# Optimization experiments

Hardware: AMD Instinct MI355X
Metric: run time of the kernel (lower is better)

The kernel has to match this reference:

```python
import jax, jax.numpy as jnp
import numpy as np

SLOPE = (1.0 / 8 + 1.0 / 3) / 2  # F.rrelu in eval mode: mean of (lower, upper)
DILS = [1, 2, 4, 8, 16]
WINDOW = 32
TEMP = 0.1


def rrelu(x):
    return jnp.where(x >= 0, x, x * SLOPE)


def conv1d(x, w, b, dil):
    # x: [B, Cin, T], w: [Cout, Cin, K]
    y = jax.lax.conv_general_dilated(x, w, window_strides=(1,), padding='VALID',
                                     rhs_dilation=(dil,),
                                     dimension_numbers=('NCH', 'OIH', 'NCH'))
    return y + b[None, :, None]


def setup_inputs() -> dict:
    key = jax.random.key(0)
    ks = jax.random.split(key, 32)
    B, T, R, K, W = 16, 16384, 8, 2, WINDOW
    ins = [1, 64, 64, 64, 64]
    outs = [64, 64, 64, 64, R]
    inp = {"x": jax.random.normal(ks[0], (B, 1, T), jnp.float32)}
    for l in range(5):
        inp[f"cw{l}"] = jax.random.normal(ks[1 + l], (outs[l], ins[l], K), jnp.float32) * 0.1
        inp[f"cb{l}"] = jax.random.normal(ks[6 + l], (outs[l],), jnp.float32) * 0.1
    pc = [(2 * R, 2 * R), (2 * R, 2 * R), (1, 2 * R)]  # params_convs, kernel 1
    for i, (o, ci) in enumerate(pc):
        inp[f"mw{i}"] = jax.random.normal(ks[11 + i], (o, ci, 1), jnp.float32) * 0.1
        inp[f"mb{i}"] = jax.random.normal(ks[14 + i], (o,), jnp.float32) * 0.1
    inp["sqrt_cov_tt"] = jax.random.uniform(ks[17], (R, 1), jnp.float32)
    inp["fish_jt"] = jax.random.normal(ks[18], (R, W), jnp.float32) * 0.01
    u = jax.random.uniform(ks[19], (B, T, R), jnp.float32, minval=1e-6, maxval=1.0 - 1e-6)
    inp["gumbel"] = -jnp.log(-jnp.log(u))
    return inp


def reference(x, cw0, cb0, cw1, cb1, cw2, cb2, cw3, cb3, cw4, cb4,
              mw0, mb0, mw1, mb1, mw2, mb2, sqrt_cov_tt, fish_jt, gumbel):
    pad = sum(DILS)
    T = x.shape[-1]
    W = WINDOW
    # forward_pass: causal dilated conv stack with rrelu
    h = jnp.pad(x, ((0, 0), (0, 0), (pad, 0)))
    for w, b, d in zip([cw0, cw1, cw2, cw3, cw4], [cb0, cb1, cb2, cb3, cb4], DILS):
        h = rrelu(conv1d(h, w, b, d))
    # h: [B, R, T]
    logits = jnp.transpose(h, (0, 2, 1))  # [B, T, R]
    gen_z = jax.nn.softmax((logits + gumbel) / TEMP, axis=-1)
    gen_z = jnp.transpose(gen_z, (0, 2, 1))  # [B, R, T]
    # params_convs (1x1 convs): conv -> (rrelu, conv) x2
    m = conv1d(jnp.concatenate([gen_z, h], axis=1), mw0, mb0, 1)
    m = conv1d(rrelu(m), mw1, mb1, 1)
    mus = conv1d(rrelu(m), mw2, mb2, 1)  # [B, 1, T]
    cov_tt = jnp.einsum('brt,rl->blt', gen_z, sqrt_cov_tt) ** 2  # [B, 1, T]
    cov_tt = cov_tt[:, :, W:T]  # [B, 1, T-W]
    fj = jnp.einsum('brt,rw->bwt', gen_z, fish_jt)[:, :, W:T]  # [B, W, T-W]
    # vectorized sliding window: x_window[b, j, t] = x[b, 0, t + j]
    idx = jnp.arange(W)[:, None] + jnp.arange(T - W)[None, :]  # [W, T-W]
    xw = x[:, 0, :][:, idx]   # [B, W, T-W]
    mw_ = mus[:, 0, :][:, idx]  # [B, W, T-W]
    _mus = mus[:, 0, W:T] - jnp.einsum('bwt,bwt->bt', cov_tt * fj, xw - mw_)
    return (_mus, gen_z)
```

## Files before the change

kernel.cpp:

```cpp
#include <hip/hip_runtime.h>
#include <hip/hip_bf16.h>

#define NT 512
#define TS 160
#define TC 192
#define NTILE 103
#define PBA 222
#define PBB 220
#define NB 16
#define T_ 16384
#define W_ 32
#define TW_ (T_ - W_)
#define SLOPE_C 0.22916666666666666f

#define WIMG_W4   49152
#define WIMG_CST  53248
#define WIMG_USH  56320

typedef short v8s __attribute__((ext_vector_type(8)));
typedef float v4f __attribute__((ext_vector_type(4)));

__device__ __forceinline__ float rr(float v){ return v >= 0.f ? v : v * SLOPE_C; }
__device__ __forceinline__ ushort f2bs(float f){ __hip_bfloat16 h = __float2bfloat16(f); return *(ushort*)&h; }
__device__ __forceinline__ float bs2f(ushort u){ union{unsigned i; float f;} v; v.i = ((unsigned)u) << 16; return v.f; }

__device__ __forceinline__ int agr(int p, int gi){ return p*128 + ((gi ^ (p & 15)) << 3); }
__device__ __forceinline__ int widx(int wr, int ci){
  return wr*64 + ((((ci >> 3) ^ (wr & 7)) << 3) | (ci & 7));
}

__global__ __launch_bounds__(256) void kW(
    const float* __restrict__ cw1, const float* __restrict__ cw2,
    const float* __restrict__ cw3, const float* __restrict__ cw4,
    const float* __restrict__ cw0, const float* __restrict__ cb0,
    const float* __restrict__ cb1, const float* __restrict__ cb2,
    const float* __restrict__ cb3, const float* __restrict__ cb4,
    const float* __restrict__ mw0, const float* __restrict__ mb0,
    const float* __restrict__ mw1, const float* __restrict__ mb1,
    const float* __restrict__ mw2, const float* __restrict__ mb2,
    const float* __restrict__ fish, const float* __restrict__ sct,
    ushort* __restrict__ wimg)
{
  const int id = blockIdx.x*256 + threadIdx.x;
  if (id < 24576){
    int l = id >> 13, e = id & 8191;
    const float* src = (l == 0) ? cw1 : ((l == 1) ? cw2 : cw3);
    int c = e >> 7, rem = e & 127, ci = rem >> 1, k = rem & 1;
    float v = src[e];
    ushort h = f2bs(v), lo = f2bs(v - bs2f(h));
    int ix = widx(k*64 + c, ci);
    wimg[l*16384 + ix] = h;
    wimg[l*16384 + 8192 + ix] = lo;
  } else if (id < 25600){
    int e = id - 24576;
    int c = e >> 7, rem = e & 127, ci = rem >> 1, k = rem & 1;
    float v = cw4[e];
    ushort h = f2bs(v), lo = f2bs(v - bs2f(h));
    int ix = widx(k*16 + c, ci);
    wimg[WIMG_W4 + ix] = h;
    wimg[WIMG_W4 + 2048 + ix] = lo;
  } else if (id < 27648){
    int e = id - 25600;
    int pl = e >> 10, rem = e & 1023, k = rem >> 9, r2 = rem & 511;
    int m = 8 + (r2 >> 6), ci = r2 & 63;
    wimg[WIMG_W4 + pl*2048 + widx(k*16 + m, ci)] = 0;
  } else if (id < 29184){
    int e = id - 27648;
    float v = 0.f;
    if      (e < 256)  v = mw0[e];
    else if (e < 512)  v = mw1[e - 256];
    else if (e < 528)  v = mw2[e - 512];
    else if (e < 544)  v = mb0[e - 528];
    else if (e < 560)  v = mb1[e - 544];
    else if (e < 561)  v = mb2[0];
    else if (e >= 576 && e < 584)  v = cb4[e - 576];
    else if (e >= 592 && e < 720)  v = cw0[e - 592];
    else if (e >= 720 && e < 784)  v = cb0[e - 720];
    else if (e >= 784 && e < 848)  v = cb1[e - 784];
    else if (e >= 848 && e < 912)  v = cb2[e - 848];
    else if (e >= 912 && e < 976)  v = cb3[e - 912];
    else if (e >= 1024 && e < 1280) v = fish[e - 1024];
    else if (e >= 1280 && e < 1288) v = sct[e - 1280];
    ((float*)(wimg + WIMG_CST))[e] = v;
  }
}

template<int D, int NSRC, int NDST>
__device__ __forceinline__ void mfma_layer(const ushort* __restrict__ src,
    ushort* __restrict__ dst, const ushort* __restrict__ wlds,
    const float* __restrict__ cbias, int tid)
{
  const int wave = tid >> 6;
  if (wave >= 7) return;
  const int lane = tid & 63;
  const int n = lane & 15, quad = lane >> 4;
  const int p0 = wave * 32;

  v4f acc[8];
  const v4f vz = {0.f, 0.f, 0.f, 0.f};
#pragma unroll
  for (int i = 0; i < 8; ++i) acc[i] = vz;

#pragma unroll
  for (int tap = 0; tap < 2; ++tap){
#pragma unroll
    for (int kb = 0; kb < 2; ++kb){
      const int kg = kb*4 + quad;
      v8s wh[4], wl[4], ah[2], al[2];
#pragma unroll
      for (int mt = 0; mt < 4; ++mt){
        int wr = tap*64 + mt*16 + n;
        int base = wr*64 + ((kg ^ (wr & 7)) << 3);
        wh[mt] = *(const v8s*)(wlds + base);
        wl[mt] = *(const v8s*)(wlds + 8192 + base);
      }
#pragma unroll
      for (int nt = 0; nt < 2; ++nt){
        int p = p0 + nt*16 + n + tap*D;
        if (p >= NSRC) p = NSRC - 1;
        ah[nt] = *(const v8s*)(src + agr(p, kg));
        al[nt] = *(const v8s*)(src + agr(p, 8 + kg));
      }
#pragma unroll
      for (int nt = 0; nt < 2; ++nt)
#pragma unroll
        for (int mt = 0; mt < 4; ++mt){
          v4f a = acc[nt*4 + mt];
          a = __builtin_amdgcn_mfma_f32_16x16x32_bf16(wh[mt], ah[nt], a, 0, 0, 0);
          a = __builtin_amdgcn_mfma_f32_16x16x32_bf16(wh[mt], al[nt], a, 0, 0, 0);
          a = __builtin_amdgcn_mfma_f32_16x16x32_bf16(wl[mt], ah[nt], a, 0, 0, 0);
          acc[nt*4 + mt] = a;
        }
    }
  }

#pragma unroll
  for (int nt = 0; nt < 2; ++nt){
    int p = p0 + nt*16 + n;
    if (p < NDST){
#pragma unroll
      for (int mt = 0; mt < 4; ++mt){
#pragma unroll
        for (int r = 0; r < 4; r += 2){
          int c = mt*16 + quad*4 + r;
          float y0 = rr(acc[nt*4 + mt][r]     + cbias[c]);
          float y1 = rr(acc[nt*4 + mt][r + 1] + cbias[c + 1]);
          ushort h0 = f2bs(y0), h1 = f2bs(y1);
          ushort l0 = f2bs(y0 - bs2f(h0)), l1 = f2bs(y1 - bs2f(h1));
          int gh = agr(p, c >> 3)       + (c & 7);
          int gl = agr(p, 8 + (c >> 3)) + (c & 7);
          *(unsigned*)(dst + gh) = (unsigned)h0 | ((unsigned)h1 << 16);
          *(unsigned*)(dst + gl) = (unsigned)l0 | ((unsigned)l1 << 16);
        }
      }
    }
  }
}

__global__ __launch_bounds__(NT) void kAB(
    const float* __restrict__ x, const float* __restrict__ gum,
    const ushort* __restrict__ wimg,
    float* __restrict__ out0, float* __restrict__ out_gz)
{
  __shared__ __align__(16) ushort bufA[PBA*128];
  __shared__ __align__(16) ushort bufB[PBB*128];
  __shared__ __align__(16) ushort wlds[16384];
  __shared__ __align__(16) ushort w4lds[4096];
  __shared__ __align__(16) float  cstl[1536];

  float* xbuf = (float*)bufB;
  float*  fA   = (float*)bufA;
  float*  h4s  = fA;
  float*  musl = fA + 1536;
  float*  pacc = fA + 1728;
  float*  xg   = fA + 2240;
  ushort* zl   = (ushort*)(fA + 2464);

  const int tile = blockIdx.x, b = blockIdx.y;
  const int o0 = tile * TS;
  const int core = (T_ - o0 < TC) ? (T_ - o0) : TC;
  const int ncut = (TW_ - o0 < TS) ? (TW_ - o0) : TS;
  const int tid = threadIdx.x;

  const int nx = core + 31;
  for (int i = tid; i < nx; i += NT){
    int g = o0 + i;
    xbuf[i] = (g >= 31) ? x[(size_t)b*T_ + g - 31] : 0.f;
  }
  for (int i = tid; i < 2048; i += NT)
    *(v8s*)(wlds + i*8) = *(const v8s*)(wimg + i*8);
  for (int i = tid; i < 512; i += NT)
    *(v8s*)(w4lds + i*8) = *(const v8s*)(wimg + WIMG_W4 + i*8);
  for (int i = tid; i < 768; i += NT)
    ((float2*)cstl)[i] = ((const float2*)(wimg + WIMG_CST))[i];
  __syncthreads();

  {
    const int n0 = core + 30;
    for (int i = tid; i < PBA*32; i += NT){
      int p = i >> 5, c = (i & 31)*2;
      float y0 = 0.f, y1 = 0.f;
      if (p < n0){
        float xp = xbuf[p], xq = xbuf[p + 1];
        y0 = rr(cstl[720 + c]     + cstl[592 + 2*c]*xp     + cstl[593 + 2*c]*xq);
        y1 = rr(cstl[720 + c + 1] + cstl[594 + 2*c]*xp     + cstl[595 + 2*c]*xq);
      }
      ushort h0 = f2bs(y0), h1 = f2bs(y1);
      ushort l0 = f2bs(y0 - bs2f(h0)), l1 = f2bs(y1 - bs2f(h1));
      *(unsigned*)(bufA + agr(p, c >> 3)       + (c & 7)) = (unsigned)h0 | ((unsigned)h1 << 16);
      *(unsigned*)(bufA + agr(p, 8 + (c >> 3)) + (c & 7)) = (unsigned)l0 | ((unsigned)l1 << 16);
    }
  }
  __syncthreads();

  mfma_layer<2, PBA, PBB>(bufA, bufB, wlds, cstl + 784, tid);
  __syncthreads();
  for (int i = tid; i < 2048; i += NT)
    *(v8s*)(wlds + i*8) = *(const v8s*)(wimg + 16384 + i*8);
  __syncthreads();
  mfma_layer<4, PBB, PBA>(bufB, bufA, wlds, cstl + 848, tid);
  __syncthreads();
  for (int i = tid; i < 2048; i += NT)
    *(v8s*)(wlds + i*8) = *(const v8s*)(wimg + 32768 + i*8);
  __syncthreads();
  mfma_layer<8, PBA, PBB>(bufA, bufB, wlds, cstl + 912, tid);
  __syncthreads();

  {
    const int wave = tid >> 6;
    if (wave < 7){
      const int lane = tid & 63;
      const int n = lane & 15, quad = lane >> 4;
      const int p0 = wave * 32;
      v4f acc2[2];
      const v4f vz = {0.f, 0.f, 0.f, 0.f};
      acc2[0] = vz; acc2[1] = vz;
#pragma unroll
      for (int tap = 0; tap < 2; ++tap){
#pragma unroll
        for (int kb = 0; kb < 2; ++kb){
          const int kg = kb*4 + quad;
          int wr = tap*16 + n;
          int base = wr*64 + ((kg ^ (wr & 7)) << 3);
          v8s wh = *(const v8s*)(w4lds + base);
          v8s wl = *(const v8s*)(w4lds + 2048 + base);
#pragma unroll
          for (int nt = 0; nt < 2; ++nt){
            int p = p0 + nt*16 + n + tap*16;
            if (p >= PBB) p = PBB - 1;
            v8s ah = *(const v8s*)(bufB + agr(p, kg));
            v8s al = *(const v8s*)(bufB + agr(p, 8 + kg));
            v4f a = acc2[nt];
            a = __builtin_amdgcn_mfma_f32_16x16x32_bf16(wh, ah, a, 0, 0, 0);
            a = __builtin_amdgcn_mfma_f32_16x16x32_bf16(wh, al, a, 0, 0, 0);
            a = __builtin_amdgcn_mfma_f32_16x16x32_bf16(wl, ah, a, 0, 0, 0);
            acc2[nt] = a;
          }
        }
      }
#pragma unroll
      for (int nt = 0; nt < 2; ++nt){
        int p = p0 + nt*16 + n;
        if (p < core && quad < 2){
#pragma unroll
          for (int r = 0; r < 4; ++r){
            int c = quad*4 + r;
            h4s[c*TC + p] = rr(acc2[nt][r] + cstl[576 + c]);
          }
        }
      }
    }
  }
  __syncthreads();

  if (tid < core){
    const int j = tid, t = o0 + j;
    float l[8];
#pragma unroll
    for (int r = 0; r < 8; ++r) l[r] = h4s[r*TC + j];
    float gv[8];
    *(float4*)&gv[0] = *(const float4*)(gum + (size_t)(b*T_ + t)*8);
    *(float4*)&gv[4] = *(const float4*)(gum + (size_t)(b*T_ + t)*8 + 4);
    float s[8], mx = -1e30f;
#pragma unroll
    for (int r = 0; r < 8; ++r){ s[r] = (l[r] + gv[r]) * 10.0f; mx = fmaxf(mx, s[r]); }
    float e[8], sum = 0.f;
#pragma unroll
    for (int r = 0; r < 8; ++r){ e[r] = __expf(s[r] - mx); sum += e[r]; }
    float inv = 1.0f / sum;
    float z[8];
#pragma unroll
    for (int r = 0; r < 8; ++r){
      z[r] = e[r] * inv;
      out_gz[(size_t)(b*8 + r)*T_ + t] = z[r];
    }
#pragma unroll
    for (int r = 0; r < 8; r += 2)
      *(unsigned*)(zl + j*8 + r) = (unsigned)f2bs(z[r]) | ((unsigned)f2bs(z[r+1]) << 16);
    float m0[16];
#pragma unroll
    for (int o = 0; o < 16; ++o){
      float a = cstl[528 + o];
#pragma unroll
      for (int i = 0; i < 8; ++i) a += cstl[o*16 + i] * z[i];
#pragma unroll
      for (int i = 0; i < 8; ++i) a += cstl[o*16 + 8 + i] * l[i];
      m0[o] = rr(a);
    }
    float m1[16];
#pragma unroll
    for (int o = 0; o < 16; ++o){
      float a = cstl[544 + o];
#pragma unroll
      for (int i = 0; i < 16; ++i) a += cstl[256 + o*16 + i] * m0[i];
      m1[o] = rr(a);
    }
    float mu = cstl[560];
#pragma unroll
    for (int i = 0; i < 16; ++i) mu += cstl[512 + i] * m1[i];
    musl[j] = mu;
  } else if (tid >= 256 && tid < 480){
    int k = tid - 256;
    int g = o0 + k;
    xg[k] = (g < T_) ? x[(size_t)b*T_ + g] : 0.f;
  }
  __syncthreads();

  {
    const int h = tid >> 8, i = tid & 255;
    if (i < ncut){
      float z[8];
      v8s zv = *(const v8s*)(zl + (i + 32)*8);
#pragma unroll
      for (int r = 0; r < 8; ++r) z[r] = bs2f((ushort)zv[r]);
      float acc = 0.f;
      const int w0 = h*16;
#pragma unroll
      for (int w = 0; w < 16; ++w){
        float fj = 0.f;
#pragma unroll
        for (int r = 0; r < 8; ++r) fj += z[r] * cstl[1024 + r*32 + w0 + w];
        acc += fj * (xg[i + w0 + w] - musl[i + w0 + w]);
      }
      pacc[h*256 + i] = acc;
    }
  }
  __syncthreads();

  if (tid < ncut){
    const int i = tid;
    float z[8];
    v8s zv = *(const v8s*)(zl + (i + 32)*8);
#pragma unroll
    for (int r = 0; r < 8; ++r) z[r] = bs2f((ushort)zv[r]);
    float cv = 0.f;
#pragma unroll
    for (int r = 0; r < 8; ++r) cv += cstl[1280 + r] * z[r];
    cv *= cv;
    float acc = pacc[i] + pacc[256 + i];
    out0[(size_t)b*TW_ + o0 + i] = musl[i + 32] - cv * acc;
  }
}

extern "C" void kernel_launch(void* const* d_in, const int* in_sizes, int n_in,
                              void* d_out, int out_size, void* d_ws, size_t ws_size,
                              hipStream_t stream)
{
  const float* x   = (const float*)d_in[0];
  const float* cw0 = (const float*)d_in[1];
  const float* cb0 = (const float*)d_in[2];
  const float* cw1 = (const float*)d_in[3];
  const float* cb1 = (const float*)d_in[4];
  const float* cw2 = (const float*)d_in[5];
  const float* cb2 = (const float*)d_in[6];
  const float* cw3 = (const float*)d_in[7];
  const float* cb3 = (const float*)d_in[8];
  const float* cw4 = (const float*)d_in[9];
  const float* cb4 = (const float*)d_in[10];
  const float* mw0 = (const float*)d_in[11];
  const float* mb0 = (const float*)d_in[12];
  const float* mw1 = (const float*)d_in[13];
  const float* mb1 = (const float*)d_in[14];
  const float* mw2 = (const float*)d_in[15];
  const float* mb2 = (const float*)d_in[16];
  const float* sct = (const float*)d_in[17];
  const float* fish= (const float*)d_in[18];
  const float* gum = (const float*)d_in[19];

  float* out0   = (float*)d_out;
  float* out_gz = out0 + NB*TW_;
  ushort* wimg  = (ushort*)d_ws;

  kW<<<114, 256, 0, stream>>>(cw1, cw2, cw3, cw4, cw0, cb0, cb1, cb2, cb3, cb4,
                              mw0, mb0, mw1, mb1, mw2, mb2, fish, sct, wimg);

  dim3 gA(NTILE, NB);
  kAB<<<gA, NT, 0, stream>>>(x, gum, wimg, out0, out_gz);
}
```

Before: 249.7 us.

## Split fused kernel into conv/softmax kernel and separate sliding-window kernel, smaller tiles

The single fused kernel is split in two. The first runs the conv stack, softmax and 1x1 MLP on smaller 96-step tiles with 256 threads, reads conv weights straight from global memory instead of staging them in LDS, and writes mus to workspace. A second kernel does the 32-wide sliding-window correction, reading gen_z and mus from global memory. This lowers LDS use, cuts halo overhead per tile and raises occupancy, at the cost of an extra launch, a global round-trip for mus and gen_z, and unswizzled global weight loads. The halo grows relative to tile size, so redundant conv work increases.

```diff
diff --git a/kernel.cpp b/kernel.cpp
--- a/kernel.cpp
+++ b/kernel.cpp
@@ -1,12 +1,11 @@
 #include <hip/hip_runtime.h>
 #include <hip/hip_bf16.h>
 
-#define NT 512
-#define TS 160
-#define TC 192
-#define NTILE 103
-#define PBA 222
-#define PBB 220
+#define NT 256
+#define TT 96
+#define NTILE 171
+#define PBA 126
+#define PBB 124
 #define NB 16
 #define T_ 16384
 #define W_ 32
@@ -25,9 +24,6 @@
 __device__ __forceinline__ float bs2f(ushort u){ union{unsigned i; float f;} v; v.i = ((unsigned)u) << 16; return v.f; }
 
 __device__ __forceinline__ int agr(int p, int gi){ return p*128 + ((gi ^ (p & 15)) << 3); }
-__device__ __forceinline__ int widx(int wr, int ci){
-  return wr*64 + ((((ci >> 3) ^ (wr & 7)) << 3) | (ci & 7));
-}
 
 __global__ __launch_bounds__(256) void kW(
     const float* __restrict__ cw1, const float* __restrict__ cw2,
@@ -48,7 +44,7 @@
     int c = e >> 7, rem = e & 127, ci = rem >> 1, k = rem & 1;
     float v = src[e];
     ushort h = f2bs(v), lo = f2bs(v - bs2f(h));
-    int ix = widx(k*64 + c, ci);
+    int ix = (k*64 + c)*64 + ci;
     wimg[l*16384 + ix] = h;
     wimg[l*16384 + 8192 + ix] = lo;
   } else if (id < 25600){
@@ -56,14 +52,14 @@
     int c = e >> 7, rem = e & 127, ci = rem >> 1, k = rem & 1;
     float v = cw4[e];
     ushort h = f2bs(v), lo = f2bs(v - bs2f(h));
-    int ix = widx(k*16 + c, ci);
+    int ix = (k*16 + c)*64 + ci;
     wimg[WIMG_W4 + ix] = h;
     wimg[WIMG_W4 + 2048 + ix] = lo;
   } else if (id < 27648){
     int e = id - 25600;
     int pl = e >> 10, rem = e & 1023, k = rem >> 9, r2 = rem & 511;
     int m = 8 + (r2 >> 6), ci = r2 & 63;
-    wimg[WIMG_W4 + pl*2048 + widx(k*16 + m, ci)] = 0;
+    wimg[WIMG_W4 + pl*2048 + (k*16 + m)*64 + ci] = 0;
   } else if (id < 29184){
     int e = id - 27648;
     float v = 0.f;
@@ -87,11 +83,10 @@
 
 template<int D, int NSRC, int NDST>
 __device__ __forceinline__ void mfma_layer(const ushort* __restrict__ src,
-    ushort* __restrict__ dst, const ushort* __restrict__ wlds,
+    ushort* __restrict__ dst, const ushort* __restrict__ wg,
     const float* __restrict__ cbias, int tid)
 {
   const int wave = tid >> 6;
-  if (wave >= 7) return;
   const int lane = tid & 63;
   const int n = lane & 15, quad = lane >> 4;
   const int p0 = wave * 32;
@@ -109,10 +104,9 @@
       v8s wh[4], wl[4], ah[2], al[2];
 #pragma unroll
       for (int mt = 0; mt < 4; ++mt){
-        int wr = tap*64 + mt*16 + n;
-        int base = wr*64 + ((kg ^ (wr & 7)) << 3);
-        wh[mt] = *(const v8s*)(wlds + base);
-        wl[mt] = *(const v8s*)(wlds + 8192 + base);
+        int base = (tap*64 + mt*16 + n)*64 + kg*8;
+        wh[mt] = *(const v8s*)(wg + base);
+        wl[mt] = *(const v8s*)(wg + 8192 + base);
       }
 #pragma unroll
       for (int nt = 0; nt < 2; ++nt){
@@ -147,39 +141,29 @@
           float y1 = rr(acc[nt*4 + mt][r + 1] + cbias[c + 1]);
           ushort h0 = f2bs(y0), h1 = f2bs(y1);
           ushort l0 = f2bs(y0 - bs2f(h0)), l1 = f2bs(y1 - bs2f(h1));
-          int gh = agr(p, c >> 3)       + (c & 7);
-          int gl = agr(p, 8 + (c >> 3)) + (c & 7);
-          *(unsigned*)(dst + gh) = (unsigned)h0 | ((unsigned)h1 << 16);
-          *(unsigned*)(dst + gl) = (unsigned)l0 | ((unsigned)l1 << 16);
+          *(unsigned*)(dst + agr(p, c >> 3)       + (c & 7)) = (unsigned)h0 | ((unsigned)h1 << 16);
+          *(unsigned*)(dst + agr(p, 8 + (c >> 3)) + (c & 7)) = (unsigned)l0 | ((unsigned)l1 << 16);
         }
       }
     }
   }
 }
 
-__global__ __launch_bounds__(NT) void kAB(
+__global__ __launch_bounds__(NT, 2) void kA(
     const float* __restrict__ x, const float* __restrict__ gum,
     const ushort* __restrict__ wimg,
-    float* __restrict__ out0, float* __restrict__ out_gz)
+    float* __restrict__ ws_mus, float* __restrict__ out_gz)
 {
   __shared__ __align__(16) ushort bufA[PBA*128];
   __shared__ __align__(16) ushort bufB[PBB*128];
-  __shared__ __align__(16) ushort wlds[16384];
-  __shared__ __align__(16) ushort w4lds[4096];
   __shared__ __align__(16) float  cstl[1536];
 
   float* xbuf = (float*)bufB;
-  float*  fA   = (float*)bufA;
-  float*  h4s  = fA;
-  float*  musl = fA + 1536;
-  float*  pacc = fA + 1728;
-  float*  xg   = fA + 2240;
-  ushort* zl   = (ushort*)(fA + 2464);
+  float* h4s  = (float*)bufA;
 
   const int tile = blockIdx.x, b = blockIdx.y;
-  const int o0 = tile * TS;
-  const int core = (T_ - o0 < TC) ? (T_ - o0) : TC;
-  const int ncut = (TW_ - o0 < TS) ? (TW_ - o0) : TS;
+  const int o0 = tile * TT;
+  const int core = (T_ - o0 < TT) ? (T_ - o0) : TT;
   const int tid = threadIdx.x;
 
   const int nx = core + 31;
@@ -187,10 +171,6 @@
     int g = o0 + i;
     xbuf[i] = (g >= 31) ? x[(size_t)b*T_ + g - 31] : 0.f;
   }
-  for (int i = tid; i < 2048; i += NT)
-    *(v8s*)(wlds + i*8) = *(const v8s*)(wimg + i*8);
-  for (int i = tid; i < 512; i += NT)
-    *(v8s*)(w4lds + i*8) = *(const v8s*)(wimg + WIMG_W4 + i*8);
   for (int i = tid; i < 768; i += NT)
     ((float2*)cstl)[i] = ((const float2*)(wimg + WIMG_CST))[i];
   __syncthreads();
@@ -202,8 +182,8 @@
       float y0 = 0.f, y1 = 0.f;
       if (p < n0){
         float xp = xbuf[p], xq = xbuf[p + 1];
-        y0 = rr(cstl[720 + c]     + cstl[592 + 2*c]*xp     + cstl[593 + 2*c]*xq);
-        y1 = rr(cstl[720 + c + 1] + cstl[594 + 2*c]*xp     + cstl[595 + 2*c]*xq);
+        y0 = rr(cstl[720 + c]     + cstl[592 + 2*c]*xp + cstl[593 + 2*c]*xq);
+        y1 = rr(cstl[720 + c + 1] + cstl[594 + 2*c]*xp + cstl[595 + 2*c]*xq);
       }
       ushort h0 = f2bs(y0), h1 = f2bs(y1);
       ushort l0 = f2bs(y0 - bs2f(h0)), l1 = f2bs(y1 - bs2f(h1));
@@ -213,60 +193,53 @@
   }
   __syncthreads();
 
-  mfma_layer<2, PBA, PBB>(bufA, bufB, wlds, cstl + 784, tid);
-  __syncthreads();
-  for (int i = tid; i < 2048; i += NT)
-    *(v8s*)(wlds + i*8) = *(const v8s*)(wimg + 16384 + i*8);
-  __syncthreads();
-  mfma_layer<4, PBB, PBA>(bufB, bufA, wlds, cstl + 848, tid);
-  __syncthreads();
-  for (int i = tid; i < 2048; i += NT)
-    *(v8s*)(wlds + i*8) = *(const v8s*)(wimg + 32768 + i*8);
-  __syncthreads();
-  mfma_layer<8, PBA, PBB>(bufA, bufB, wlds, cstl + 912, tid);
+  mfma_layer<2, PBA, PBB>(bufA, bufB, wimg,         cstl + 784, tid);
+  __syncthreads();
+  mfma_layer<4, PBB, 120>(bufB, bufA, wimg + 16384, cstl + 848, tid);
+  __syncthreads();
+  mfma_layer<8, 120, 112>(bufA, bufB, wimg + 32768, cstl + 912, tid);
   __syncthreads();
 
   {
+    const ushort* wg4 = wimg + WIMG_W4;
     const int wave = tid >> 6;
-    if (wave < 7){
-      const int lane = tid & 63;
-      const int n = lane & 15, quad = lane >> 4;
-      const int p0 = wave * 32;
-      v4f acc2[2];
-      const v4f vz = {0.f, 0.f, 0.f, 0.f};
-      acc2[0] = vz; acc2[1] = vz;
-#pragma unroll
-      for (int tap = 0; tap < 2; ++tap){
-#pragma unroll
-        for (int kb = 0; kb < 2; ++kb){
-          const int kg = kb*4 + quad;
-          int wr = tap*16 + n;
-          int base = wr*64 + ((kg ^ (wr & 7)) << 3);
-          v8s wh = *(const v8s*)(w4lds + base);
-          v8s wl = *(const v8s*)(w4lds + 2048 + base);
-#pragma unroll
-          for (int nt = 0; nt < 2; ++nt){
-            int p = p0 + nt*16 + n + tap*16;
-            if (p >= PBB) p = PBB - 1;
-            v8s ah = *(const v8s*)(bufB + agr(p, kg));
-            v8s al = *(const v8s*)(bufB + agr(p, 8 + kg));
-            v4f a = acc2[nt];
-            a = __builtin_amdgcn_mfma_f32_16x16x32_bf16(wh, ah, a, 0, 0, 0);
-            a = __builtin_amdgcn_mfma_f32_16x16x32_bf16(wh, al, a, 0, 0, 0);
-            a = __builtin_amdgcn_mfma_f32_16x16x32_bf16(wl, ah, a, 0, 0, 0);
-            acc2[nt] = a;
-          }
+    const int lane = tid & 63;
+    const int n = lane & 15, quad = lane >> 4;
+    const int p0 = wave * 32;
+    v4f acc2[2];
+    const v4f vz = {0.f, 0.f, 0.f, 0.f};
+    acc2[0] = vz; acc2[1] = vz;
+#pragma unroll
+    for (int tap = 0; tap < 2; ++tap){
+#pragma unroll
+      for (int kb = 0; kb < 2; ++kb){
+        const int kg = kb*4 + quad;
+        int base = (tap*16 + n)*64 + kg*8;
+        v8s wh = *(const v8s*)(wg4 + base);
+        v8s wl = *(const v8s*)(wg4 + 2048 + base);
+#pragma unroll
+        for (int nt = 0; nt < 2; ++nt){
+          int p = p0 + nt*16 + n + tap*16;
+          if (p >= 112) p = 111;
+          v8s ah = *(const v8s*)(bufB + agr(p, kg));
+          v8s al = *(const v8s*)(bufB + agr(p, 8 + kg));
+          v4f a = acc2[nt];
+          a = __builtin_amdgcn_mfma_f32_16x16x32_bf16(wh, ah, a, 0, 0, 0);
+          a = __builtin_amdgcn_mfma_f32_16x16x32_bf16(wh, al, a, 0, 0, 0);
+          a = __builtin_amdgcn_mfma_f32_16x16x32_bf16(wl, ah, a, 0, 0, 0);
+          acc2[nt] = a;
         }
       }
-#pragma unroll
-      for (int nt = 0; nt < 2; ++nt){
-        int p = p0 + nt*16 + n;
-        if (p < core && quad < 2){
-#pragma unroll
-          for (int r = 0; r < 4; ++r){
-            int c = quad*4 + r;
-            h4s[c*TC + p] = rr(acc2[nt][r] + cstl[576 + c]);
-          }
+    }
+    __syncthreads();
+#pragma unroll
+    for (int nt = 0; nt < 2; ++nt){
+      int p = p0 + nt*16 + n;
+      if (p < core && quad < 2){
+#pragma unroll
+        for (int r = 0; r < 4; ++r){
+          int c = quad*4 + r;
+          h4s[c*TT + p] = rr(acc2[nt][r] + cstl[576 + c]);
         }
       }
     }
@@ -274,10 +247,10 @@
   __syncthreads();
 
   if (tid < core){
-    const int j = tid, t = o0 + j;
+    const int t = o0 + tid;
     float l[8];
 #pragma unroll
-    for (int r = 0; r < 8; ++r) l[r] = h4s[r*TC + j];
+    for (int r = 0; r < 8; ++r) l[r] = h4s[r*TT + tid];
     float gv[8];
     *(float4*)&gv[0] = *(const float4*)(gum + (size_t)(b*T_ + t)*8);
     *(float4*)&gv[4] = *(const float4*)(gum + (size_t)(b*T_ + t)*8 + 4);
@@ -294,9 +267,6 @@
       z[r] = e[r] * inv;
       out_gz[(size_t)(b*8 + r)*T_ + t] = z[r];
     }
-#pragma unroll
-    for (int r = 0; r < 8; r += 2)
-      *(unsigned*)(zl + j*8 + r) = (unsigned)f2bs(z[r]) | ((unsigned)f2bs(z[r+1]) << 16);
     float m0[16];
 #pragma unroll
     for (int o = 0; o < 16; ++o){
@@ -318,47 +288,47 @@
     float mu = cstl[560];
 #pragma unroll
     for (int i = 0; i < 16; ++i) mu += cstl[512 + i] * m1[i];
-    musl[j] = mu;
-  } else if (tid >= 256 && tid < 480){
-    int k = tid - 256;
-    int g = o0 + k;
-    xg[k] = (g < T_) ? x[(size_t)b*T_ + g] : 0.f;
-  }
-  __syncthreads();
-
-  {
-    const int h = tid >> 8, i = tid & 255;
-    if (i < ncut){
-      float z[8];
-      v8s zv = *(const v8s*)(zl + (i + 32)*8);
-#pragma unroll
-      for (int r = 0; r < 8; ++r) z[r] = bs2f((ushort)zv[r]);
-      float acc = 0.f;
-      const int w0 = h*16;
-#pragma unroll
-      for (int w = 0; w < 16; ++w){
-        float fj = 0.f;
-#pragma unroll
-        for (int r = 0; r < 8; ++r) fj += z[r] * cstl[1024 + r*32 + w0 + w];
-        acc += fj * (xg[i + w0 + w] - musl[i + w0 + w]);
-      }
-      pacc[h*256 + i] = acc;
-    }
-  }
-  __syncthreads();
-
-  if (tid < ncut){
-    const int i = tid;
+    ws_mus[(size_t)b*T_ + t] = mu;
+  }
+}
+
+__global__ __launch_bounds__(256) void kB(
+    const float* __restrict__ x, const float* __restrict__ fish,
+    const float* __restrict__ sct, const float* __restrict__ ws_mus,
+    const float* __restrict__ gz, float* __restrict__ out0)
+{
+  __shared__ float xm[288], mm[288], fs[256], sc[8];
+  const int b = blockIdx.y;
+  const int s = blockIdx.x * 256;
+  const int tid = threadIdx.x;
+  for (int i = tid; i < 288; i += 256){
+    int g = s + i;
+    bool ok = g < T_;
+    xm[i] = ok ? x[(size_t)b*T_ + g] : 0.f;
+    mm[i] = ok ? ws_mus[(size_t)b*T_ + g] : 0.f;
+  }
+  fs[tid] = fish[tid];
+  if (tid < 8) sc[tid] = sct[tid];
+  __syncthreads();
+  const int tp = s + tid;
+  if (tp < TW_){
+    const int t = W_ + tp;
     float z[8];
-    v8s zv = *(const v8s*)(zl + (i + 32)*8);
-#pragma unroll
-    for (int r = 0; r < 8; ++r) z[r] = bs2f((ushort)zv[r]);
+#pragma unroll
+    for (int r = 0; r < 8; ++r) z[r] = gz[(size_t)(b*8 + r)*T_ + t];
     float cv = 0.f;
 #pragma unroll
-    for (int r = 0; r < 8; ++r) cv += cstl[1280 + r] * z[r];
+    for (int r = 0; r < 8; ++r) cv += sc[r] * z[r];
     cv *= cv;
-    float acc = pacc[i] + pacc[256 + i];
-    out0[(size_t)b*TW_ + o0 + i] = musl[i + 32] - cv * acc;
+    float acc = 0.f;
+#pragma unroll 4
+    for (int w = 0; w < 32; ++w){
+      float fj = 0.f;
+#pragma unroll
+      for (int r = 0; r < 8; ++r) fj += z[r] * fs[r*32 + w];
+      acc += fj * (xm[tid + w] - mm[tid + w]);
+    }
+    out0[(size_t)b*TW_ + tp] = mm[tid + 32] - cv * acc;
   }
 }
 
@@ -390,10 +360,13 @@
   float* out0   = (float*)d_out;
   float* out_gz = out0 + NB*TW_;
   ushort* wimg  = (ushort*)d_ws;
+  float* ws_mus = (float*)((char*)d_ws + 131072);
 
   kW<<<114, 256, 0, stream>>>(cw1, cw2, cw3, cw4, cw0, cb0, cb1, cb2, cb3, cb4,
                               mw0, mb0, mw1, mb1, mw2, mb2, fish, sct, wimg);
 
   dim3 gA(NTILE, NB);
-  kAB<<<gA, NT, 0, stream>>>(x, gum, wimg, out0, out_gz);
-}
+  kA<<<gA, NT, 0, stream>>>(x, gum, wimg, ws_mus, out_gz);
+  dim3 gB((TW_ + 255) / 256, NB);
+  kB<<<gB, 256, 0, stream>>>(x, fish, sct, ws_mus, out_gz, out0);
+}
```

Result: slower. 302.2 us (+21.0%).
